# Kernel tuning notes

Measured on AMD Instinct MI355X. Metric: run time of the kernel, lower is better.

The kernel has to match this reference:

```python
import jax, jax.numpy as jnp
from jax import lax
import numpy as np

B, C, H, W = 8, 64, 56, 56
LM = 9              # level_map: NSCT subbands per channel
D = LM * C + C      # 640: swin block dim
DEPTH = 2
WIN = 7
HEADS = 8
KS = 5              # NSCT filter kernel size


def _nsct_filters():
    # fixed nonsubsampled 9-band filter bank (lowpass + 8 directional), stand-in for myNSCTd
    r = np.arange(KS) - KS // 2
    yy, xx = np.meshgrid(r, r, indexing='ij')
    g = np.exp(-(xx ** 2 + yy ** 2) / 4.0)
    g = g / g.sum()
    f = [g]
    for k in range(LM - 1):
        th = k * np.pi / (LM - 1)
        d = (np.cos(th) * xx + np.sin(th) * yy) * g
        d = d - d.mean()
        d = d / np.sqrt((d ** 2).sum())
        f.append(d)
    return jnp.asarray(np.stack(f), dtype=jnp.float32)  # [LM,KS,KS]


def _ct(x):
    # per-(b,c) NSCT decomposition -> [B, LM*C, H, W], band-major (matches transpose(0,2,1,3,4).reshape)
    Bx, Cx, Hx, Wx = x.shape
    K = _nsct_filters()
    k = jnp.tile(K, (Cx, 1, 1))[:, None]  # [Cx*LM,1,KS,KS], out channel index c*LM+band
    o = lax.conv_general_dilated(x, k, (1, 1), 'SAME',
                                 dimension_numbers=('NCHW', 'OIHW', 'NCHW'),
                                 feature_group_count=Cx)
    o = o.reshape(Bx, Cx, LM, Hx, Wx).transpose(0, 2, 1, 3, 4).reshape(Bx, LM * Cx, Hx, Wx)
    return o


def _ict(y):
    # inverse transform: reshape(B,LM,C,H,W).permute(0,2,1,3,4), reconstruct per channel
    Bx = y.shape[0]
    t = y.reshape(Bx, LM, C, H, W).transpose(0, 2, 1, 3, 4).reshape(Bx, C * LM, H, W)
    K = _nsct_filters()
    g = jnp.broadcast_to(K, (C, LM, KS, KS))  # groups=C: 9 subbands -> 1 channel each
    return lax.conv_general_dilated(t, g, (1, 1), 'SAME',
                                    dimension_numbers=('NCHW', 'OIHW', 'NCHW'),
                                    feature_group_count=C)


def _ln(x, g, b):
    m = x.mean(-1, keepdims=True)
    v = x.var(-1, keepdims=True)
    return (x - m) / jnp.sqrt(v + 1e-5) * g + b


def _attn_mask(shift):
    # standard SW-MSA mask for shifted windows
    img = np.zeros((H, W), np.int32)
    c = 0
    for hs in (slice(0, -WIN), slice(-WIN, -shift), slice(-shift, None)):
        for ws in (slice(0, -WIN), slice(-WIN, -shift), slice(-shift, None)):
            img[hs, ws] = c
            c += 1
    a = img.reshape(H // WIN, WIN, W // WIN, WIN).transpose(0, 2, 1, 3).reshape(-1, WIN * WIN)
    m = np.where(a[:, :, None] != a[:, None, :], -1e9, 0.0).astype(np.float32)
    return jnp.asarray(m)  # [nWindows, T, T]


def _swin_block(x, p, shift):
    Bx = x.shape[0]
    T = WIN * WIN
    dh = D // HEADS
    nH, nWw = H // WIN, W // WIN
    sc = x
    h = _ln(x, p['ln1_g'], p['ln1_b'])
    if shift:
        h = jnp.roll(h, (-shift, -shift), (1, 2))
    w = h.reshape(Bx, nH, WIN, nWw, WIN, D).transpose(0, 1, 3, 2, 4, 5).reshape(Bx * nH * nWw, T, D)
    qkv = w @ p['qkv_w'] + p['qkv_b']
    q, k, v = jnp.split(qkv, 3, axis=-1)
    heads = lambda t: t.reshape(-1, T, HEADS, dh).transpose(0, 2, 1, 3)
    q, k, v = heads(q), heads(k), heads(v)
    s = jnp.einsum('nhtd,nhsd->nhts', q, k) / jnp.sqrt(jnp.asarray(dh, x.dtype))
    if shift:
        m = _attn_mask(shift)
        s = (s.reshape(Bx, nH * nWw, HEADS, T, T) + m[None, :, None]).reshape(-1, HEADS, T, T)
    a = jax.nn.softmax(s, -1)
    o = jnp.einsum('nhts,nhsd->nhtd', a, v).transpose(0, 2, 1, 3).reshape(-1, T, D)
    o = o @ p['proj_w'] + p['proj_b']
    o = o.reshape(Bx, nH, nWw, WIN, WIN, D).transpose(0, 1, 3, 2, 4, 5).reshape(Bx, H, W, D)
    if shift:
        o = jnp.roll(o, (shift, shift), (1, 2))
    x = sc + o
    h2 = _ln(x, p['ln2_g'], p['ln2_b'])
    h2 = jax.nn.gelu(h2 @ p['fc1_w'] + p['fc1_b']) @ p['fc2_w'] + p['fc2_b']
    return x + h2


def setup_inputs() -> dict:
    key = jax.random.key(0)
    ks = jax.random.split(key, 8)
    s = 0.02
    n = lambda k, shp: jax.random.normal(k, shp, jnp.float32) * s
    return {
        'x': jax.random.normal(ks[0], (B, C, H, W), jnp.float32),
        'ln1_g': jnp.ones((DEPTH, D), jnp.float32), 'ln1_b': jnp.zeros((DEPTH, D), jnp.float32),
        'qkv_w': n(ks[1], (DEPTH, D, 3 * D)), 'qkv_b': jnp.zeros((DEPTH, 3 * D), jnp.float32),
        'proj_w': n(ks[2], (DEPTH, D, D)), 'proj_b': jnp.zeros((DEPTH, D), jnp.float32),
        'ln2_g': jnp.ones((DEPTH, D), jnp.float32), 'ln2_b': jnp.zeros((DEPTH, D), jnp.float32),
        'fc1_w': n(ks[3], (DEPTH, D, 4 * D)), 'fc1_b': jnp.zeros((DEPTH, 4 * D), jnp.float32),
        'fc2_w': n(ks[4], (DEPTH, 4 * D, D)), 'fc2_b': jnp.zeros((DEPTH, D), jnp.float32),
        'lin_w': n(ks[5], (D, LM * C)), 'lin_b': jnp.zeros((LM * C,), jnp.float32),
        'conv_w': n(ks[6], (C, D)), 'conv_b': jnp.zeros((C,), jnp.float32),
    }


def reference(x, ln1_g, ln1_b, qkv_w, qkv_b, proj_w, proj_b, ln2_g, ln2_b,
              fc1_w, fc1_b, fc2_w, fc2_b, lin_w, lin_b, conv_w, conv_b):
    x2 = jax.nn.relu(x)
    x_trans = lax.stop_gradient(_ct(x2))          # CT detaches its input in the original
    x3 = jnp.concatenate([x_trans, x2], axis=1)   # [B, 10C, H, W]
    x3 = x3.transpose(0, 2, 3, 1)                 # BHWC
    for i in range(DEPTH):
        p = dict(ln1_g=ln1_g[i], ln1_b=ln1_b[i], qkv_w=qkv_w[i], qkv_b=qkv_b[i],
                 proj_w=proj_w[i], proj_b=proj_b[i], ln2_g=ln2_g[i], ln2_b=ln2_b[i],
                 fc1_w=fc1_w[i], fc1_b=fc1_b[i], fc2_w=fc2_w[i], fc2_b=fc2_b[i])
        x3 = _swin_block(x3, p, 0 if i % 2 == 0 else WIN // 2)
    x3 = x3 @ lin_w + lin_b                        # D -> LM*C
    y = x3.transpose(0, 3, 1, 2)                   # [B, 9C, H, W]
    y_trans = lax.stop_gradient(_ict(y))           # ICT detaches its input in the original
    yc = jnp.concatenate([y_trans, y], axis=1)     # [B, 10C, H, W]
    out = jnp.einsum('bchw,oc->bohw', yc, conv_w) + conv_b[None, :, None, None]
    return out
```

## Files before the change

kernel.cpp:

```cpp
#include <hip/hip_runtime.h>
#include <hip/hip_bf16.h>
#include <math.h>

typedef __attribute__((ext_vector_type(4))) float f32x4;
typedef __attribute__((ext_vector_type(8))) short short8;

#define NTOK 25088
#define DD   640

__device__ __forceinline__ void gload_lds16(const void* g, void* l) {
    __builtin_amdgcn_global_load_lds((const __attribute__((address_space(1))) void*)g,
                                     (__attribute__((address_space(3))) void*)l,
                                     16, 0, 0);
}

__device__ __forceinline__ float gelu_f(float t) {
    float u = 1.5957691216057308f * (t + 0.044715f * t * t * t);
    float e = __builtin_amdgcn_exp2f(u * -1.4426950408889634f);
    return t / (1.f + e);
}

__global__ void init_consts(float* __restrict__ filt, float* __restrict__ linbp,
                            const float* __restrict__ lin_b, float* __restrict__ convbp,
                            const float* __restrict__ conv_b) {
    int t = threadIdx.x;
    if (t == 0) {
        float g[25]; float s = 0.f;
        for (int i = 0; i < 5; i++) for (int j = 0; j < 5; j++) {
            float yy = (float)(i - 2), xx = (float)(j - 2);
            float v = expf(-(xx*xx + yy*yy) * 0.25f);
            g[i*5+j] = v; s += v;
        }
        for (int i = 0; i < 25; i++) { g[i] /= s; filt[i] = g[i]; }
        for (int k = 0; k < 8; k++) {
            float th = (float)k * 3.14159265358979323846f / 8.f;
            float ct = cosf(th), st = sinf(th);
            float d[25]; float mean = 0.f;
            for (int i = 0; i < 5; i++) for (int j = 0; j < 5; j++) {
                float yy = (float)(i - 2), xx = (float)(j - 2);
                d[i*5+j] = (ct*xx + st*yy) * g[i*5+j];
                mean += d[i*5+j];
            }
            mean *= (1.f/25.f);
            float ss = 0.f;
            for (int i = 0; i < 25; i++) { d[i] -= mean; ss += d[i]*d[i]; }
            ss = sqrtf(ss);
            for (int i = 0; i < 25; i++) filt[(k+1)*25 + i] = d[i] / ss;
        }
    }
    for (int i = t; i < 640; i += 256) linbp[i]  = (i < 576) ? lin_b[i]  : 0.f;
    for (int i = t; i < 128; i += 256) convbp[i] = (i < 64)  ? conv_b[i] : 0.f;
}

__global__ __launch_bounds__(256)
void wtrans_kernel(const float* __restrict__ src, __hip_bfloat16* __restrict__ dst,
                   int K, int Nsrc) {
    __shared__ float tile[32][33];
    const int n0 = blockIdx.x * 32;
    const int k0 = blockIdx.y * 32;
    const int tx = threadIdx.x, ty = threadIdx.y;
    #pragma unroll
    for (int r = ty; r < 32; r += 8) {
        int k = k0 + r, n = n0 + tx;
        tile[r][tx] = (n < Nsrc) ? src[(long)k * Nsrc + n] : 0.f;
    }
    __syncthreads();
    #pragma unroll
    for (int r = ty; r < 32; r += 8) {
        int n = n0 + r, k = k0 + tx;
        dst[(long)n * K + k] = __float2bfloat16(tile[tx][r]);
    }
}

__global__ void wcast_kernel(const float* __restrict__ src, __hip_bfloat16* __restrict__ dst,
                             int count, int total) {
    int i = blockIdx.x * 256 + threadIdx.x;
    if (i < total) dst[i] = __float2bfloat16(i < count ? src[i] : 0.f);
}

__global__ __launch_bounds__(256)
void prep_kernel(const float* __restrict__ x, const float* __restrict__ filt,
                 float* __restrict__ x3) {
    __shared__ float sf[225];
    for (int i = threadIdx.x; i < 225; i += 256) sf[i] = filt[i];
    __syncthreads();
    int id = blockIdx.x * 256 + threadIdx.x;
    int c = id & 63;
    int pix = id >> 6;
    int w = pix % 56, h = (pix / 56) % 56, b = pix / 3136;
    const float* xp = x + (long)(b * 64 + c) * 3136;
    float nb[25];
    #pragma unroll
    for (int dy = 0; dy < 5; dy++) {
        int hy = h + dy - 2;
        #pragma unroll
        for (int dx = 0; dx < 5; dx++) {
            int wx = w + dx - 2;
            float v = 0.f;
            if (hy >= 0 && hy < 56 && wx >= 0 && wx < 56) v = fmaxf(xp[hy*56 + wx], 0.f);
            nb[dy*5 + dx] = v;
        }
    }
    float* orow = x3 + (long)pix * DD;
    #pragma unroll
    for (int band = 0; band < 9; band++) {
        float a = 0.f;
        #pragma unroll
        for (int t = 0; t < 25; t++) a += nb[t] * sf[band*25 + t];
        orow[band*64 + c] = a;
    }
    orow[576 + c] = nb[12];
}

__global__ __launch_bounds__(256)
void ln_kernel(const float* __restrict__ xin, const float* __restrict__ g,
               const float* __restrict__ bt, __hip_bfloat16* __restrict__ out) {
    const int lane = threadIdx.x & 63;
    const long tok = (long)blockIdx.x * 4 + (threadIdx.x >> 6);
    const float* xr = xin + tok * DD;
    float v[10]; float s = 0.f, s2 = 0.f;
    #pragma unroll
    for (int i = 0; i < 10; i++) { float t = xr[lane + (i << 6)]; v[i] = t; s += t; s2 += t*t; }
    #pragma unroll
    for (int o = 32; o > 0; o >>= 1) { s += __shfl_down(s, o); s2 += __shfl_down(s2, o); }
    s = __shfl(s, 0); s2 = __shfl(s2, 0);
    const float mean = s * (1.f/640.f);
    const float var  = s2 * (1.f/640.f) - mean * mean;
    const float inv  = 1.f / sqrtf(var + 1e-5f);
    __hip_bfloat16* orow = out + tok * DD;
    #pragma unroll
    for (int i = 0; i < 10; i++) {
        int c = lane + (i << 6);
        orow[c] = __float2bfloat16((v[i] - mean) * inv * g[c] + bt[c]);
    }
}

__global__ __launch_bounds__(256, 2)
void gemm128_kernel(const __hip_bfloat16* __restrict__ A,
                    const __hip_bfloat16* __restrict__ Bt,
                    const float* __restrict__ bias,
                    const float* __restrict__ resid,
                    float* __restrict__ Cf,
                    __hip_bfloat16* __restrict__ Cb,
                    int K, int ldc, int ncf, int ldb, int col_off, int ncb,
                    int act_gelu, int nvalid, int mode) {
    extern __shared__ __align__(16) char smraw[];
    __hip_bfloat16* sm = (__hip_bfloat16*)smraw;

    const int tid  = threadIdx.x;
    const int lane = tid & 63;
    const int wv   = tid >> 6;
    const int wr   = wv >> 1;
    const int wc   = wv & 1;

    const int gx   = gridDim.x;
    const int nwg  = gx * gridDim.y;
    const int orig = blockIdx.y * gx + blockIdx.x;
    const int qq = nwg >> 3, rr = nwg & 7;
    const int xcd = orig & 7, lid = orig >> 3;
    const int wg = (xcd < rr ? xcd * (qq + 1) : rr * (qq + 1) + (xcd - rr) * qq) + lid;
    const long m0 = (long)(wg / gx) * 128;
    const long n0 = (long)(wg % gx) * 128;

    const bool wact = ((int)n0 + (wc << 6)) < nvalid;

    f32x4 acc[4][4];
    #pragma unroll
    for (int i = 0; i < 4; i++)
        #pragma unroll
        for (int j = 0; j < 4; j++) acc[i][j] = (f32x4){0.f, 0.f, 0.f, 0.f};

    const int srow  = tid >> 3;
    const int slot  = tid & 7;
    const int sslot = slot ^ (srow & 7);
    const __hip_bfloat16* Agb = A  + (m0 + srow) * (long)K + (sslot << 3);
    const __hip_bfloat16* Bgb = Bt + (n0 + srow) * (long)K + (sslot << 3);
    __hip_bfloat16* dA = sm + srow * 64 + (slot << 3);
    __hip_bfloat16* dB = sm + 8192 + srow * 64 + (slot << 3);

    const int frow = lane & 15;
    const int fks  = lane >> 4;

    auto STAGE = [&](int b, int k0) {
        #pragma unroll
        for (int i = 0; i < 4; i++) {
            gload_lds16(Agb + (long)i * 32 * K + k0, dA + b * 16384 + i * 2048);
            gload_lds16(Bgb + (long)i * 32 * K + k0, dB + b * 16384 + i * 2048);
        }
    };

    const int nt = K >> 6;
    STAGE(0, 0);
    for (int t = 0; t < nt; ++t) {
        const int cur = t & 1;
        if (t + 1 < nt) {
            STAGE(cur ^ 1, (t + 1) << 6);
            asm volatile("s_waitcnt vmcnt(8)" ::: "memory");
        } else {
            asm volatile("s_waitcnt vmcnt(0)" ::: "memory");
        }
        __builtin_amdgcn_s_barrier();
        __builtin_amdgcn_sched_barrier(0);

        const __hip_bfloat16* pA = sm + cur * 16384;
        const __hip_bfloat16* pB = sm + 8192 + cur * 16384;
        if (wact) {
            #pragma unroll
            for (int ks = 0; ks < 2; ++ks) {
                short8 af[4], bfr[4];
                #pragma unroll
                for (int mi = 0; mi < 4; ++mi) {
                    const int R = (wr << 6) + (mi << 4) + frow;
                    af[mi] = *(const short8*)(pA + R * 64 + ((((ks << 2) | fks) ^ (R & 7)) << 3));
                }
                #pragma unroll
                for (int nj = 0; nj < 4; ++nj) {
                    const int Rn = (wc << 6) + (nj << 4) + frow;
                    bfr[nj] = *(const short8*)(pB + Rn * 64 + ((((ks << 2) | fks) ^ (Rn & 7)) << 3));
                }
                __builtin_amdgcn_s_setprio(1);
                #pragma unroll
                for (int mi = 0; mi < 4; ++mi)
                    #pragma unroll
                    for (int nj = 0; nj < 4; ++nj)
                        acc[mi][nj] = __builtin_amdgcn_mfma_f32_16x16x32_bf16(
                            bfr[nj], af[mi], acc[mi][nj], 0, 0, 0);
                __builtin_amdgcn_s_setprio(0);
            }
        }
        asm volatile("" ::: "memory");
        __builtin_amdgcn_s_barrier();
    }

    if (!wact) return;
    const int nlim = (ncf > ncb) ? ncf : ncb;
    #pragma unroll
    for (int mi = 0; mi < 4; ++mi) {
        const long row = m0 + (wr << 6) + (mi << 4) + frow;
        #pragma unroll
        for (int nj = 0; nj < 4; ++nj) {
            const int n = (int)n0 + (wc << 6) + (nj << 4) + (fks << 2);
            if (n >= nlim) continue;
            f32x4 v = acc[mi][nj];
            if (bias) {
                const f32x4 bv = *(const f32x4*)&bias[n];
                v += bv;
            }
            if (act_gelu) {
                v[0] = gelu_f(v[0]); v[1] = gelu_f(v[1]); v[2] = gelu_f(v[2]); v[3] = gelu_f(v[3]);
            }
            if (mode == 1) {
                const int b = (int)(row / 3136), pos = (int)(row % 3136);
                #pragma unroll
                for (int r = 0; r < 4; ++r)
                    Cf[(long)(b * 64 + n + r) * 3136 + pos] = v[r];
                continue;
            }
            if (resid && n < ncf) v += *(const f32x4*)&resid[row * (long)ldc + n];
            if (Cf && n < ncf) *(f32x4*)&Cf[row * (long)ldc + n] = v;
            if (Cb && n < ncb) {
                short4 p;
                p.x = (short)__bfloat16_as_short(__float2bfloat16(v[0]));
                p.y = (short)__bfloat16_as_short(__float2bfloat16(v[1]));
                p.z = (short)__bfloat16_as_short(__float2bfloat16(v[2]));
                p.w = (short)__bfloat16_as_short(__float2bfloat16(v[3]));
                *(short4*)&Cb[row * (long)ldb + col_off + n] = p;
            }
        }
    }
}

__global__ __launch_bounds__(256)
void attn_kernel(const __hip_bfloat16* __restrict__ qkv, __hip_bfloat16* __restrict__ o,
                 int shift) {
    __shared__ __align__(16) float qT[80][52];
    __shared__ __align__(16) float kT[80][52];
    __shared__ __align__(16) float vs[50][80];
    __shared__ __align__(16) float ss[49][52];
    __shared__ int toks[49];
    __shared__ int rid[49];

    const int tid = threadIdx.x;
    const int win = blockIdx.x >> 3;
    const int hd  = blockIdx.x & 7;
    const int b   = win >> 6;
    const int wh  = (win >> 3) & 7;
    const int ww  = win & 7;

    if (tid < 49) {
        int i = tid / 7, j = tid % 7;
        int ph = wh * 7 + i, pw = ww * 7 + j;
        int sh = ph + shift; if (sh >= 56) sh -= 56;
        int sw = pw + shift; if (sw >= 56) sw -= 56;
        toks[tid] = (b * 56 + sh) * 56 + sw;
        int rh = (ph < 49) ? 0 : ((ph < 53) ? 1 : 2);
        int rw = (pw < 49) ? 0 : ((pw < 53) ? 1 : 2);
        rid[tid] = rh * 3 + rw;
    }
    for (int i = tid; i < 80 * 3; i += 256) {
        int d = i / 3, cc = 49 + (i % 3);
        qT[d][cc] = 0.f; kT[d][cc] = 0.f;
    }
    __syncthreads();
    for (int idx = tid; idx < 49 * 80; idx += 256) {
        int t = idx / 80, d = idx % 80;
        long base = (long)toks[t] * 1920 + hd * 80 + d;
        qT[d][t] = __bfloat162float(qkv[base]);
        kT[d][t] = __bfloat162float(qkv[base + 640]);
        vs[t][d] = __bfloat162float(qkv[base + 1280]);
    }
    __syncthreads();
    const float scale = 0.11180339887498948f;
    for (int p = tid; p < 49 * 13; p += 256) {
        int t = p / 13, j0 = (p % 13) * 4;
        float4 a = {0.f, 0.f, 0.f, 0.f};
        #pragma unroll
        for (int d = 0; d < 80; d++) {
            float qv = qT[d][t];
            float4 kv = *(const float4*)&kT[d][j0];
            a.x += qv * kv.x; a.y += qv * kv.y; a.z += qv * kv.z; a.w += qv * kv.w;
        }
        a.x *= scale; a.y *= scale; a.z *= scale; a.w *= scale;
        *(float4*)&ss[t][j0] = a;
    }
    __syncthreads();
    if (tid < 49) {
        const int myr = rid[tid];
        float mx = -1e30f;
        for (int j = 0; j < 49; j++) {
            float v = ss[tid][j];
            if (shift && rid[j] != myr) v = -1e9f;
            ss[tid][j] = v;
            mx = fmaxf(mx, v);
        }
        float sum = 0.f;
        for (int j = 0; j < 49; j++) {
            float e = expf(ss[tid][j] - mx);
            ss[tid][j] = e; sum += e;
        }
        float inv = 1.f / sum;
        for (int j = 0; j < 49; j++) ss[tid][j] *= inv;
    }
    __syncthreads();
    for (int p = tid; p < 49 * 20; p += 256) {
        int t = p / 20, dv = (p % 20) * 4;
        float4 a = {0.f, 0.f, 0.f, 0.f};
        for (int j = 0; j < 49; j++) {
            float w = ss[t][j];
            float4 vv = *(const float4*)&vs[j][dv];
            a.x += w * vv.x; a.y += w * vv.y; a.z += w * vv.z; a.w += w * vv.w;
        }
        long base = (long)toks[t] * DD + hd * 80 + dv;
        o[base + 0] = __float2bfloat16(a.x);
        o[base + 1] = __float2bfloat16(a.y);
        o[base + 2] = __float2bfloat16(a.z);
        o[base + 3] = __float2bfloat16(a.w);
    }
}

__global__ __launch_bounds__(256)
void ict_kernel(const float* __restrict__ y, const float* __restrict__ filt,
                __hip_bfloat16* __restrict__ ayc) {
    __shared__ float sf[225];
    for (int i = threadIdx.x; i < 225; i += 256) sf[i] = filt[i];
    __syncthreads();
    int id = blockIdx.x * 256 + threadIdx.x;
    int c = id & 63;
    int pix = id >> 6;
    int w = pix % 56, h = (pix / 56) % 56, b = pix / 3136;
    float a = 0.f;
    #pragma unroll
    for (int dy = 0; dy < 5; dy++) {
        int hy = h + dy - 2;
        if (hy < 0 || hy >= 56) continue;
        #pragma unroll
        for (int dx = 0; dx < 5; dx++) {
            int wx = w + dx - 2;
            if (wx < 0 || wx >= 56) continue;
            const float* yr = y + ((long)(b * 56 + hy) * 56 + wx) * DD + c;
            #pragma unroll
            for (int band = 0; band < 9; band++)
                a += yr[band * 64] * sf[band*25 + dy*5 + dx];
        }
    }
    ayc[(long)pix * DD + c] = __float2bfloat16(a);
}

extern "C" void kernel_launch(void* const* d_in, const int* in_sizes, int n_in,
                              void* d_out, int out_size, void* d_ws, size_t ws_size,
                              hipStream_t stream) {
    (void)in_sizes; (void)n_in; (void)out_size; (void)ws_size;
    const float* x      = (const float*)d_in[0];
    const float* ln1_g  = (const float*)d_in[1];
    const float* ln1_b  = (const float*)d_in[2];
    const float* qkv_w  = (const float*)d_in[3];
    const float* qkv_b  = (const float*)d_in[4];
    const float* proj_w = (const float*)d_in[5];
    const float* proj_b = (const float*)d_in[6];
    const float* ln2_g  = (const float*)d_in[7];
    const float* ln2_b  = (const float*)d_in[8];
    const float* fc1_w  = (const float*)d_in[9];
    const float* fc1_b  = (const float*)d_in[10];
    const float* fc2_w  = (const float*)d_in[11];
    const float* fc2_b  = (const float*)d_in[12];
    const float* lin_w  = (const float*)d_in[13];
    const float* lin_b  = (const float*)d_in[14];
    const float* conv_w = (const float*)d_in[15];
    const float* conv_b = (const float*)d_in[16];

    char* ws = (char*)d_ws;
    size_t off = 0;
    auto alloc = [&](size_t bytes) -> void* {
        void* p = ws + off;
        off += (bytes + 255) & ~(size_t)255;
        return p;
    };
    float* filt   = (float*)alloc(225 * 4);
    float* linbp  = (float*)alloc(640 * 4);
    float* convbp = (float*)alloc(128 * 4);
    __hip_bfloat16* qkvWt[2], *projWt[2], *fc1Wt[2], *fc2Wt[2];
    for (int i = 0; i < 2; i++) qkvWt[i] = (__hip_bfloat16*)alloc(1920L * 640 * 2);
    for (int i = 0; i < 2; i++) projWt[i] = (__hip_bfloat16*)alloc(640L * 640 * 2);
    for (int i = 0; i < 2; i++) fc1Wt[i] = (__hip_bfloat16*)alloc(2560L * 640 * 2);
    for (int i = 0; i < 2; i++) fc2Wt[i] = (__hip_bfloat16*)alloc(640L * 2560 * 2);
    __hip_bfloat16* linWt  = (__hip_bfloat16*)alloc(640L * 640 * 2);
    __hip_bfloat16* convWt = (__hip_bfloat16*)alloc(128L * 640 * 2);
    float* x3 = (float*)alloc((long)NTOK * DD * 4);
    __hip_bfloat16* bufA = (__hip_bfloat16*)alloc((long)NTOK * DD * 2);
    char* bufB = (char*)alloc((long)NTOK * 2560 * 2);
    __hip_bfloat16* qkv = (__hip_bfloat16*)bufB;
    __hip_bfloat16* h2  = (__hip_bfloat16*)bufB;
    float* ybuf = (float*)bufB;
    __hip_bfloat16* ayc = (__hip_bfloat16*)(bufB + (long)NTOK * DD * 4);

    hipFuncSetAttribute((const void*)gemm128_kernel,
                        hipFuncAttributeMaxDynamicSharedMemorySize, 65536);

    dim3 tb(32, 8);
    init_consts<<<1, 256, 0, stream>>>(filt, linbp, lin_b, convbp, conv_b);
    for (int i = 0; i < 2; i++) {
        wtrans_kernel<<<dim3(60, 20), tb, 0, stream>>>(qkv_w + (long)i*640*1920, qkvWt[i], 640, 1920);
        wtrans_kernel<<<dim3(20, 20), tb, 0, stream>>>(proj_w + (long)i*640*640,  projWt[i], 640, 640);
        wtrans_kernel<<<dim3(80, 20), tb, 0, stream>>>(fc1_w + (long)i*640*2560, fc1Wt[i], 640, 2560);
        wtrans_kernel<<<dim3(20, 80), tb, 0, stream>>>(fc2_w + (long)i*2560*640, fc2Wt[i], 2560, 640);
    }
    wtrans_kernel<<<dim3(20, 20), tb, 0, stream>>>(lin_w, linWt, 640, 576);
    wcast_kernel<<<320, 256, 0, stream>>>(conv_w, convWt, 64 * 640, 128 * 640);

    prep_kernel<<<6272, 256, 0, stream>>>(x, filt, x3);

    for (int i = 0; i < 2; i++) {
        int shift = i ? 3 : 0;
        ln_kernel<<<6272, 256, 0, stream>>>(x3, ln1_g + i*640, ln1_b + i*640, bufA);
        gemm128_kernel<<<dim3(15, 196), 256, 65536, stream>>>(bufA, qkvWt[i], qkv_b + i*1920,
            nullptr, nullptr, qkv, 640, 0, 0, 1920, 0, 1920, 0, 1920, 0);
        attn_kernel<<<4096, 256, 0, stream>>>(qkv, bufA, shift);
        gemm128_kernel<<<dim3(5, 196), 256, 65536, stream>>>(bufA, projWt[i], proj_b + i*640,
            x3, x3, nullptr, 640, 640, 640, 0, 0, 0, 0, 640, 0);
        ln_kernel<<<6272, 256, 0, stream>>>(x3, ln2_g + i*640, ln2_b + i*640, bufA);
        gemm128_kernel<<<dim3(20, 196), 256, 65536, stream>>>(bufA, fc1Wt[i], fc1_b + i*2560,
            nullptr, nullptr, h2, 640, 0, 0, 2560, 0, 2560, 1, 2560, 0);
        gemm128_kernel<<<dim3(5, 196), 256, 65536, stream>>>(h2, fc2Wt[i], fc2_b + i*640,
            x3, x3, (i == 1) ? bufA : nullptr, 2560, 640, 640, 640, 0, (i == 1) ? 640 : 0, 0, 640, 0);
    }
    gemm128_kernel<<<dim3(5, 196), 256, 65536, stream>>>(bufA, linWt, linbp,
        nullptr, ybuf, ayc, 640, 640, 640, 640, 64, 576, 0, 576, 0);
    ict_kernel<<<6272, 256, 0, stream>>>(ybuf, filt, ayc);
    gemm128_kernel<<<dim3(1, 196), 256, 65536, stream>>>(ayc, convWt, convbp,
        nullptr, (float*)d_out, nullptr, 640, 0, 64, 0, 0, 0, 0, 64, 1);
}
```

Before: 1.489 ms.

## Unroll GEMM double-buffer loop, parallelize softmax rows, vectorize ICT kernel

The GEMM main loop is manually unrolled by two so the buffer offsets become compile-time constants. The attention softmax now spreads each row over 4 threads using shuffle reductions and fast exp, where before a single thread handled each of the 49 rows. The ICT kernel now computes 4 channels per thread with float4 loads and a packed bf16 store, with the grid reduced to match. Together these target address arithmetic, serial softmax latency and scalar memory traffic. The costs are more code size and a different exp accuracy.

Result: faster. 1.442 ms (-3.2%).

```diff
diff --git a/kernel.cpp b/kernel.cpp
--- a/kernel.cpp
+++ b/kernel.cpp
@@ -180,6 +180,7 @@
 
     const int frow = lane & 15;
     const int fks  = lane >> 4;
+    const int fr7  = frow & 7;
 
     auto STAGE = [&](int b, int k0) {
         #pragma unroll
@@ -189,48 +190,65 @@
         }
     };
 
+#define COMPUTE(BUFOFF)                                                                     \
+    do {                                                                                    \
+        const __hip_bfloat16* pA = sm + (BUFOFF);                                           \
+        const __hip_bfloat16* pB = sm + 8192 + (BUFOFF);                                    \
+        if (wact) {                                                                         \
+            _Pragma("unroll")                                                               \
+            for (int ks = 0; ks < 2; ++ks) {                                                \
+                short8 af[4], bfr[4];                                                       \
+                _Pragma("unroll")                                                           \
+                for (int mi = 0; mi < 4; ++mi) {                                            \
+                    const int R = (wr << 6) + (mi << 4) + frow;                             \
+                    af[mi] = *(const short8*)(pA + R * 64 +                                 \
+                              ((((ks << 2) | fks) ^ (R & 7)) << 3));                        \
+                }                                                                           \
+                _Pragma("unroll")                                                           \
+                for (int nj = 0; nj < 4; ++nj) {                                            \
+                    const int Rn = (wc << 6) + (nj << 4) + frow;                            \
+                    bfr[nj] = *(const short8*)(pB + Rn * 64 +                               \
+                               ((((ks << 2) | fks) ^ (Rn & 7)) << 3));                      \
+                }                                                                           \
+                __builtin_amdgcn_s_setprio(1);                                              \
+                _Pragma("unroll")                                                           \
+                for (int mi = 0; mi < 4; ++mi)                                              \
+                    _Pragma("unroll")                                                       \
+                    for (int nj = 0; nj < 4; ++nj)     \
+                        acc[mi][nj] = __builtin_amdgcn_mfma_f32_16x16x32_bf16(              \
+                            bfr[nj], af[mi], acc[mi][nj], 0, 0, 0);                         \
+                __builtin_amdgcn_s_setprio(0);                                              \
+            }                                                                               \
+        }                                                                                   \
+    } while (0)
+
     const int nt = K >> 6;
     STAGE(0, 0);
-    for (int t = 0; t < nt; ++t) {
-        const int cur = t & 1;
-        if (t + 1 < nt) {
-            STAGE(cur ^ 1, (t + 1) << 6);
+    for (int t2 = 0; t2 < nt; t2 += 2) {
+        if (t2 + 1 < nt) {
+            STAGE(1, (t2 + 1) << 6);
             asm volatile("s_waitcnt vmcnt(8)" ::: "memory");
         } else {
             asm volatile("s_waitcnt vmcnt(0)" ::: "memory");
         }
         __builtin_amdgcn_s_barrier();
         __builtin_amdgcn_sched_barrier(0);
-
-        const __hip_bfloat16* pA = sm + cur * 16384;
-        const __hip_bfloat16* pB = sm + 8192 + cur * 16384;
-        if (wact) {
-            #pragma unroll
-            for (int ks = 0; ks < 2; ++ks) {
-                short8 af[4], bfr[4];
-                #pragma unroll
-                for (int mi = 0; mi < 4; ++mi) {
-                    const int R = (wr << 6) + (mi << 4) + frow;
-                    af[mi] = *(const short8*)(pA + R * 64 + ((((ks << 2) | fks) ^ (R & 7)) << 3));
-                }
-                #pragma unroll
-                for (int nj = 0; nj < 4; ++nj) {
-                    const int Rn = (wc << 6) + (nj << 4) + frow;
-                    bfr[nj] = *(const short8*)(pB + Rn * 64 + ((((ks << 2) | fks) ^ (Rn & 7)) << 3));
-                }
-                __builtin_amdgcn_s_setprio(1);
-                #pragma unroll
-                for (int mi = 0; mi < 4; ++mi)
-                    #pragma unroll
-                    for (int nj = 0; nj < 4; ++nj)
-                        acc[mi][nj] = __builtin_amdgcn_mfma_f32_16x16x32_bf16(
-                            bfr[nj], af[mi], acc[mi][nj], 0, 0, 0);
-                __builtin_amdgcn_s_setprio(0);
-            }
-        }
+        COMPUTE(0);
         asm volatile("" ::: "memory");
         __builtin_amdgcn_s_barrier();
-    }
+        if (t2 + 2 < nt) {
+            STAGE(0, (t2 + 2) << 6);
+            asm volatile("s_waitcnt vmcnt(8)" ::: "memory");
+        } else {
+            asm volatile("s_waitcnt vmcnt(0)" ::: "memory");
+        }
+        __builtin_amdgcn_s_barrier();
+        __builtin_amdgcn_sched_barrier(0);
+        COMPUTE(16384);
+        asm volatile("" ::: "memory");
+        __builtin_amdgcn_s_barrier();
+    }
+#undef COMPUTE
 
     if (!wact) return;
     const int nlim = (ncf > ncb) ? ncf : ncb;
@@ -324,22 +342,30 @@
         *(float4*)&ss[t][j0] = a;
     }
     __syncthreads();
-    if (tid < 49) {
-        const int myr = rid[tid];
+    if (tid < 196) {
+        const int r = tid >> 2, sub = tid & 3;
+        const int j0 = sub * 13;
+        const int j1 = (sub == 3) ? 10 : 13;
+        const int myr = rid[r];
         float mx = -1e30f;
-        for (int j = 0; j < 49; j++) {
-            float v = ss[tid][j];
-            if (shift && rid[j] != myr) v = -1e9f;
-            ss[tid][j] = v;
+        for (int i = 0; i < j1; i++) {
+            float v = ss[r][j0 + i];
+            if (shift && rid[j0 + i] != myr) v = -1e9f;
+            ss[r][j0 + i] = v;
             mx = fmaxf(mx, v);
         }
+        mx = fmaxf(mx, __shfl_xor(mx, 1));
+        mx = fmaxf(mx, __shfl_xor(mx, 2));
         float sum = 0.f;
-        for (int j = 0; j < 49; j++) {
-            float e = expf(ss[tid][j] - mx);
-            ss[tid][j] = e; sum += e;
-        }
-        float inv = 1.f / sum;
-        for (int j = 0; j < 49; j++) ss[tid][j] *= inv;
+        for (int i = 0; i < j1; i++) {
+            float e = __expf(ss[r][j0 + i] - mx);
+            ss[r][j0 + i] = e;
+            sum += e;
+        }
+        sum += __shfl_xor(sum, 1);
+        sum += __shfl_xor(sum, 2);
+        const float inv = 1.f / sum;
+        for (int i = 0; i < j1; i++) ss[r][j0 + i] *= inv;
     }
     __syncthreads();
     for (int p = tid; p < 49 * 20; p += 256) {
@@ -365,10 +391,10 @@
     for (int i = threadIdx.x; i < 225; i += 256) sf[i] = filt[i];
     __syncthreads();
     int id = blockIdx.x * 256 + threadIdx.x;
-    int c = id & 63;
-    int pix = id >> 6;
+    int c4 = (id & 15) << 2;
+    int pix = id >> 4;
     int w = pix % 56, h = (pix / 56) % 56, b = pix / 3136;
-    float a = 0.f;
+    float4 a = {0.f, 0.f, 0.f, 0.f};
     #pragma unroll
     for (int dy = 0; dy < 5; dy++) {
         int hy = h + dy - 2;
@@ -377,13 +403,21 @@
         for (int dx = 0; dx < 5; dx++) {
             int wx = w + dx - 2;
             if (wx < 0 || wx >= 56) continue;
-            const float* yr = y + ((long)(b * 56 + hy) * 56 + wx) * DD + c;
+            const float* yr = y + ((long)(b * 56 + hy) * 56 + wx) * DD + c4;
             #pragma unroll
-            for (int band = 0; band < 9; band++)
-                a += yr[band * 64] * sf[band*25 + dy*5 + dx];
-        }
-    }
-    ayc[(long)pix * DD + c] = __float2bfloat16(a);
+            for (int band = 0; band < 9; band++) {
+                const float f = sf[band*25 + dy*5 + dx];
+                const float4 vv = *(const float4*)&yr[band * 64];
+                a.x += vv.x * f; a.y += vv.y * f; a.z += vv.z * f; a.w += vv.w * f;
+            }
+        }
+    }
+    short4 p;
+    p.x = (short)__bfloat16_as_short(__float2bfloat16(a.x));
+    p.y = (short)__bfloat16_as_short(__float2bfloat16(a.y));
+    p.z = (short)__bfloat16_as_short(__float2bfloat16(a.z));
+    p.w = (short)__bfloat16_as_short(__float2bfloat16(a.w));
+    *(short4*)&ayc[(long)pix * DD + c4] = p;
 }
 
 extern "C" void kernel_launch(void* const* d_in, const int* in_sizes, int n_in,
@@ -465,7 +499,7 @@
     }
     gemm128_kernel<<<dim3(5, 196), 256, 65536, stream>>>(bufA, linWt, linbp,
         nullptr, ybuf, ayc, 640, 640, 640, 640, 64, 576, 0, 576, 0);
-    ict_kernel<<<6272, 256, 0, stream>>>(ybuf, filt, ayc);
+    ict_kernel<<<1568, 256, 0, stream>>>(ybuf, filt, ayc);
     gemm128_kernel<<<dim3(1, 196), 256, 65536, stream>>>(ayc, convWt, convbp,
         nullptr, (float*)d_out, nullptr, 640, 0, 64, 0, 0, 0, 0, 64, 1);
 }
```
